# Optimization experiments

Measured on AMD Instinct MI355X. Metric: run time of the kernel, lower is better.

## Reference

```python
import jax, jax.numpy as jnp
import numpy as np

N_REGIONS = 20

def setup_inputs() -> dict:
    key = jax.random.key(0)
    k0, k1 = jax.random.split(key)
    B, L, D = 64, 1024, 2048
    in0 = jax.random.normal(k0, (B * N_REGIONS, D), dtype=jnp.float32)  # region embeddings
    in1 = jax.random.normal(k1, (B, L, D), dtype=jnp.float32)           # word embeddings
    return {"in0": in0, "in1": in1}

def reference(in0, in1):
    # in0: (B*20, D) image region embeddings; in1: (B, L, D) word embeddings
    B = in1.shape[0]
    regions = in0.reshape(B, N_REGIONS, in0.shape[1])        # (B, 20, D)
    # batched_dot(regions, words^T): (B, 20, D) x (B, D, L) -> (B, 20, L)
    scores = jnp.einsum('brd,bld->brl', regions, in1)
    # max over regions, keepdims -> (B, 1, L)
    return jnp.max(scores, axis=1, keepdims=True)
```

## Files before the change

kernel.cpp:

```cpp
#include <hip/hip_runtime.h>
#include <hip/hip_bf16.h>
#include <math.h>
#include <string.h>

#define NREG   20
#define LWORDS 1024
#define DDIM   2048
#define TPB    512
#define KSTEPS (DDIM / 32)

typedef __attribute__((ext_vector_type(8))) short bf16x8;
typedef __attribute__((ext_vector_type(4))) float f32x4;
typedef __attribute__((ext_vector_type(4))) unsigned int u32x4;

__device__ __forceinline__ unsigned pk2(float lo, float hi) {
    __hip_bfloat162 h = __float22bfloat162_rn(make_float2(lo, hi));
    unsigned u;
    memcpy(&u, &h, 4);
    return u;
}

#define CVT8(bq, p0, p1)                                                       \
    do {                                                                       \
        u32x4 t_;                                                              \
        t_[0] = pk2(p0[0], p0[1]); t_[1] = pk2(p0[2], p0[3]);                  \
        t_[2] = pk2(p1[0], p1[1]); t_[3] = pk2(p1[2], p1[3]);                  \
        memcpy(&bq, &t_, 16);                                                  \
    } while (0)

#define WLOAD(va, vb, kk)                                                      \
    do {                                                                       \
        const f32x4* p_ = reinterpret_cast<const f32x4*>(                      \
            wbase + (size_t)(kk) * 32);                                        \
        va = __builtin_nontemporal_load(p_);                                   \
        vb = __builtin_nontemporal_load(p_ + 1);                               \
    } while (0)

#define CSTEP(kk, va, vb)                                                      \
    do {                                                                       \
        bf16x8 bq_; CVT8(bq_, va, vb);                                         \
        const bf16x8 a0_ = lds0[(kk) * 64 + lane];                             \
        const bf16x8 a1_ = lds1[(kk) * 16 + (col & 3) * 4 + kg];               \
        acc0 = __builtin_amdgcn_mfma_f32_16x16x32_bf16(a0_, bq_, acc0, 0, 0, 0); \
        acc1 = __builtin_amdgcn_mfma_f32_16x16x32_bf16(a1_, bq_, acc1, 0, 0, 0); \
    } while (0)

__global__ __launch_bounds__(TPB)
void score_mfma_kernel(const float* __restrict__ in0,
                       const float* __restrict__ in1,
                       float* __restrict__ out) {
    __shared__ bf16x8 lds0[KSTEPS * 64];
    __shared__ bf16x8 lds1[KSTEPS * 16];

    const int bid  = blockIdx.x;
    const int b    = bid & 63;
    const int tb   = bid >> 6;
    const int tid  = threadIdx.x;
    const int wave = tid >> 6;
    const int lane = tid & 63;
    const int col  = lane & 15;
    const int kg   = lane >> 4;

    const float* reg0 = in0 + (size_t)b * NREG * DDIM;
    const float* wbase = in1
        + ((size_t)b * LWORDS + tb * 128 + wave * 16 + col) * DDIM + kg * 8;

    f32x4 pa0, pa1, pb0, pb1;
    WLOAD(pa0, pa1, 0);
    WLOAD(pb0, pb1, 1);

    #pragma unroll
    for (int i = 0; i < 8; ++i) {
        const int S = i * TPB + tid;
        const int ks = S >> 6, l = S & 63, r = l & 15, g = l >> 4;
        const float* src = reg0 + (size_t)r * DDIM + ks * 32 + g * 8;
        const f32x4 x = *reinterpret_cast<const f32x4*>(src);
        const f32x4 y = *reinterpret_cast<const f32x4*>(src + 4);
        bf16x8 o; CVT8(o, x, y);
        lds0[S] = o;
    }
    #pragma unroll
    for (int i = 0; i < 2; ++i) {
        const int S = i * TPB + tid;
        const int ks = S >> 4, r4 = (S >> 2) & 3, g = S & 3;
        const float* src = reg0 + (size_t)(16 + r4) * DDIM + ks * 32 + g * 8;
        const f32x4 x = *reinterpret_cast<const f32x4*>(src);
        const f32x4 y = *reinterpret_cast<const f32x4*>(src + 4);
        bf16x8 o; CVT8(o, x, y);
        lds1[S] = o;
    }
    __syncthreads();

    f32x4 acc0 = {0.f, 0.f, 0.f, 0.f};
    f32x4 acc1 = {0.f, 0.f, 0.f, 0.f};

    for (int ks = 0; ks < KSTEPS - 2; ks += 2) {
        CSTEP(ks,     pa0, pa1);  WLOAD(pa0, pa1, ks + 2);
        CSTEP(ks + 1, pb0, pb1);  WLOAD(pb0, pb1, ks + 3);
    }
    CSTEP(KSTEPS - 2, pa0, pa1);
    CSTEP(KSTEPS - 1, pb0, pb1);

    float m = fmaxf(fmaxf(fmaxf(acc0[0], acc0[1]), fmaxf(acc0[2], acc0[3])),
                    fmaxf(fmaxf(acc1[0], acc1[1]), fmaxf(acc1[2], acc1[3])));
    m = fmaxf(m, __shfl_xor(m, 16, 64));
    m = fmaxf(m, __shfl_xor(m, 32, 64));
    if (lane < 16)
        out[(size_t)b * LWORDS + tb * 128 + wave * 16 + col] = m;
}

extern "C" void kernel_launch(void* const* d_in, const int* in_sizes, int n_in,
                              void* d_out, int out_size, void* d_ws, size_t ws_size,
                              hipStream_t stream) {
    const float* in0 = (const float*)d_in[0];
    const float* in1 = (const float*)d_in[1];
    float* out = (float*)d_out;

    const int grid = 64 * (LWORDS / 128);
    score_mfma_kernel<<<grid, TPB, 0, stream>>>(in0, in1, out);
}
```

Baseline: 117.2 us.

## Precompute bf16 region fragments in a prepass and DMA them into LDS

```diff
diff --git a/kernel.cpp b/kernel.cpp
--- a/kernel.cpp
+++ b/kernel.cpp
@@ -8,10 +8,18 @@
 #define DDIM   2048
 #define TPB    512
 #define KSTEPS (DDIM / 32)
+#define FRAGS  (KSTEPS * 64 + KSTEPS * 16)
 
 typedef __attribute__((ext_vector_type(8))) short bf16x8;
 typedef __attribute__((ext_vector_type(4))) float f32x4;
 typedef __attribute__((ext_vector_type(4))) unsigned int u32x4;
+
+__device__ __forceinline__ void gload_lds16(const void* src, void* dst) {
+    __builtin_amdgcn_global_load_lds(
+        (const __attribute__((address_space(1))) void*)src,
+        (__attribute__((address_space(3))) void*)dst,
+        16, 0, 0);
+}
 
 __device__ __forceinline__ unsigned pk2(float lo, float hi) {
     __hip_bfloat162 h = __float22bfloat162_rn(make_float2(lo, hi));
@@ -32,8 +40,8 @@
     do {                                                                       \
         const f32x4* p_ = reinterpret_cast<const f32x4*>(                      \
             wbase + (size_t)(kk) * 32);                                        \
-        va = __builtin_nontemporal_load(p_);                                   \
-        vb = __builtin_nontemporal_load(p_ + 1);                               \
+        va = *p_;                                                              \
+        vb = *(p_ + 1);                                                        \
     } while (0)
 
 #define CSTEP(kk, va, vb)                                                      \
@@ -44,6 +52,77 @@
         acc0 = __builtin_amdgcn_mfma_f32_16x16x32_bf16(a0_, bq_, acc0, 0, 0, 0); \
         acc1 = __builtin_amdgcn_mfma_f32_16x16x32_bf16(a1_, bq_, acc1, 0, 0, 0); \
     } while (0)
+
+__global__ __launch_bounds__(512)
+void region_prepass(const float* __restrict__ in0, bf16x8* __restrict__ wsb) {
+    const int gid = blockIdx.x * 512 + threadIdx.x;
+    const int b = gid / FRAGS;
+    const int S = gid - b * FRAGS;
+    const float* reg0 = in0 + (size_t)b * NREG * DDIM;
+    const float* src;
+    if (S < KSTEPS * 64) {
+        const int ks = S >> 6, l = S & 63, r = l & 15, g = l >> 4;
+        src = reg0 + (size_t)r * DDIM + ks * 32 + g * 8;
+    } else {
+        const int s = S - KSTEPS * 64;
+        const int ks = s >> 4, r4 = (s >> 2) & 3, g = s & 3;
+        src = reg0 + (size_t)(16 + r4) * DDIM + ks * 32 + g * 8;
+    }
+    const f32x4 x = *reinterpret_cast<const f32x4*>(src);
+    const f32x4 y = *reinterpret_cast<const f32x4*>(src + 4);
+    bf16x8 o; CVT8(o, x, y);
+    wsb[gid] = o;
+}
+
+__global__ __launch_bounds__(TPB)
+void score_mfma2(const bf16x8* __restrict__ wsb,
+                 const float* __restrict__ in1,
+                 float* __restrict__ out) {
+    __shared__ bf16x8 ldsA[FRAGS];
+    bf16x8* lds0 = ldsA;
+    bf16x8* lds1 = ldsA + KSTEPS * 64;
+
+    const int bid  = blockIdx.x;
+    const int b    = bid & 63;
+    const int tb   = bid >> 6;
+    const int tid  = threadIdx.x;
+    const int wave = tid >> 6;
+    const int lane = tid & 63;
+    const int col  = lane & 15;
+    const int kg   = lane >> 4;
+
+    const float* wbase = in1
+        + ((size_t)b * LWORDS + tb * 128 + wave * 16 + col) * DDIM + kg * 8;
+    const char* wsb_b = reinterpret_cast<const char*>(wsb + (size_t)b * FRAGS);
+
+    f32x4 pa0, pa1, pb0, pb1;
+    WLOAD(pa0, pa1, 0);
+    WLOAD(pb0, pb1, 1);
+
+    #pragma unroll
+    for (int i = 0; i < 10; ++i) {
+        const int t = i * 8 + wave;
+        gload_lds16(wsb_b + (size_t)t * 1024 + lane * 16, &ldsA[t * 64]);
+    }
+    __syncthreads();
+
+    f32x4 acc0 = {0.f, 0.f, 0.f, 0.f};
+    f32x4 acc1 = {0.f, 0.f, 0.f, 0.f};
+
+    for (int ks = 0; ks < KSTEPS - 2; ks += 2) {
+        CSTEP(ks,     pa0, pa1);  WLOAD(pa0, pa1, ks + 2);
+        CSTEP(ks + 1, pb0, pb1);  WLOAD(pb0, pb1, ks + 3);
+    }
+    CSTEP(KSTEPS - 2, pa0, pa1);
+    CSTEP(KSTEPS - 1, pb0, pb1);
+
+    float m = fmaxf(fmaxf(fmaxf(acc0[0], acc0[1]), fmaxf(acc0[2], acc0[3])),
+                    fmaxf(fmaxf(acc1[0], acc1[1]), fmaxf(acc1[2], acc1[3])));
+    m = fmaxf(m, __shfl_xor(m, 16, 64));
+    m = fmaxf(m, __shfl_xor(m, 32, 64));
+    if (lane < 16)
+        out[(size_t)b * LWORDS + tb * 128 + wave * 16 + col] = m;
+}
 
 __global__ __launch_bounds__(TPB)
 void score_mfma_kernel(const float* __restrict__ in0,
@@ -116,6 +195,14 @@
     const float* in1 = (const float*)d_in[1];
     float* out = (float*)d_out;
 
+    const size_t ws_need = (size_t)64 * FRAGS * 16;
     const int grid = 64 * (LWORDS / 128);
-    score_mfma_kernel<<<grid, TPB, 0, stream>>>(in0, in1, out);
-}
+
+    if (ws_size >= ws_need) {
+        bf16x8* wsb = (bf16x8*)d_ws;
+        region_prepass<<<(64 * FRAGS) / 512, 512, 0, stream>>>(in0, wsb);
+        score_mfma2<<<grid, TPB, 0, stream>>>(wsb, in1, out);
+    } else {
+        score_mfma_kernel<<<grid, TPB, 0, stream>>>(in0, in1, out);
+    }
+}
```

New measurement: 112.2 us. -4.3%, faster.
